# Kernel tuning notes

Hardware: AMD Instinct MI355X
Metric: run time of the kernel (lower is better)

## Reference

```python
import jax, jax.numpy as jnp
import numpy as np

NUM_NODES = 100000
NUM_EDGES = 640000
IN_DIM = 128
OUT_DIM = 128
NUM_REL = 16


def setup_inputs() -> dict:
    key = jax.random.key(0)
    k1, k2, k3, k4, k5 = jax.random.split(key, 5)
    x = jax.random.normal(k1, (NUM_NODES, IN_DIM), dtype=jnp.float32)
    edge_index = jax.random.randint(k2, (2, NUM_EDGES), 0, NUM_NODES, dtype=jnp.int64)
    edge_types = jax.random.randint(k3, (NUM_EDGES,), 0, NUM_REL, dtype=jnp.int64)
    # xavier-uniform-ish params
    rw_bound = float(np.sqrt(6.0 / (IN_DIM * OUT_DIM + NUM_REL)))
    relation_weights = jax.random.uniform(k4, (NUM_REL, IN_DIM, OUT_DIM), dtype=jnp.float32, minval=-rw_bound, maxval=rw_bound)
    sw_bound = float(np.sqrt(6.0 / (IN_DIM + OUT_DIM)))
    self_weight = jax.random.uniform(k5, (IN_DIM, OUT_DIM), dtype=jnp.float32, minval=-sw_bound, maxval=sw_bound)
    bias = jnp.zeros((OUT_DIM,), dtype=jnp.float32)
    return {
        'x': x,
        'edge_index': edge_index,
        'edge_types': edge_types,
        'relation_weights': relation_weights,
        'self_weight': self_weight,
        'bias': bias,
    }


def reference(x, edge_index, edge_types, relation_weights, self_weight, bias):
    num_nodes = x.shape[0]
    # self loop transform: (N, out)
    self_msg = x @ self_weight
    # transform all nodes by every relation weight once: (R, N, out)
    transformed = jnp.einsum('ni,rio->rno', x, relation_weights)
    src = edge_index[0]
    dst = edge_index[1]
    # per-edge message: pick (relation, source) transformed feature -> (E, out)
    msgs = transformed[edge_types, src]
    # scatter-add into destination nodes
    neighbor_msg = jax.ops.segment_sum(msgs, dst, num_segments=num_nodes)
    # dropout=0.0 (eval) -> identity
    return jax.nn.relu(self_msg + neighbor_msg + bias)
```

## Files before the change

### kernel.cpp

```cpp
#include <hip/hip_runtime.h>

#define N_NODES 100000
#define N_EDGES 640000
#define IN_DIM  128
#define OUT_DIM 128
#define N_REL   16
#define EPB     64
#define MEPB    128
#define SELF_PAD 100096
#define MAX_SLOTS (SELF_PAD + N_EDGES + 2048)
#define SENT    (N_EDGES + N_NODES)
#define MSG_ROWS (N_EDGES + N_NODES + 128)
#define NB_SCAN ((N_NODES + 255) / 256)
#define CVT_XB  (N_NODES * IN_DIM / 4 / 256)
#define CVT_WB  (17 * 16384 / 256)
#define HIST_B  ((N_EDGES + 255) / 256)
#define SELF_B  (SELF_PAD / 256)
#define MB      (MAX_SLOTS / MEPB)

typedef unsigned short u16;
typedef unsigned int   u32;
typedef __attribute__((ext_vector_type(8))) short bf16x8;
typedef __attribute__((ext_vector_type(4))) float f32x4;

__device__ inline u16 f2bf(float f) {
    u32 u = __builtin_bit_cast(u32, f);
    return (u16)((u + 0x7fffu + ((u >> 16) & 1u)) >> 16);
}
__device__ inline float bf2f(u16 s) {
    u32 u = ((u32)s) << 16;
    return __builtin_bit_cast(float, u);
}

__global__ __launch_bounds__(256) void k_pre(const float* __restrict__ x,
                                             const float* __restrict__ rw,
                                             const float* __restrict__ sw,
                                             const int* __restrict__ etype,
                                             const int* __restrict__ dst,
                                             u16* __restrict__ xb,
                                             u16* __restrict__ wt,
                                             int* __restrict__ counts_rel,
                                             int* __restrict__ dst_count,
                                             int* __restrict__ sorted) {
    int b = blockIdx.x, t = threadIdx.x;
    if (b < CVT_XB) {
        int i = b * 256 + t;
        float4 v = ((const float4*)x)[i];
        ushort4 p; p.x = f2bf(v.x); p.y = f2bf(v.y); p.z = f2bf(v.z); p.w = f2bf(v.w);
        ((ushort4*)xb)[i] = p;
    } else if (b < CVT_XB + CVT_WB) {
        int i = (b - CVT_XB) * 256 + t;
        int r = i >> 14, rem = i & 16383;
        int k = rem >> 7, np = rem & 127;
        float v = (r < 16) ? rw[i] : sw[rem];
        int c = np >> 4, nn = np & 15, kk = k >> 5, q = (k >> 3) & 3, j = k & 7;
        wt[(size_t)r * 16384 + (c * 4 + kk) * 512 + (q * 16 + nn) * 8 + j] = f2bf(v);
    } else if (b < CVT_XB + CVT_WB + HIST_B) {
        __shared__ int bins[N_REL];
        if (t < N_REL) bins[t] = 0;
        __syncthreads();
        int e = (b - CVT_XB - CVT_WB) * 256 + t;
        if (e < N_EDGES) {
            atomicAdd(&bins[etype[e]], 1);
            atomicAdd(&dst_count[dst[e]], 1);
        }
        __syncthreads();
        if (t < N_REL && bins[t]) atomicAdd(&counts_rel[t], bins[t]);
    } else {
        int i = (b - CVT_XB - CVT_WB - HIST_B) * 256 + t;
        sorted[i] = (i < N_NODES) ? (N_EDGES + i) : SENT;
    }
}

__global__ __launch_bounds__(256) void k_scan1(const int* __restrict__ dst_count,
                                               int* __restrict__ row_ptr,
                                               int* __restrict__ part) {
    __shared__ int buf[2][256];
    int t = threadIdx.x;
    int i = blockIdx.x * 256 + t;
    int v = (i < N_NODES) ? (dst_count[i] + 1) : 0;
    buf[0][t] = v;
    __syncthreads();
    int cur = 0;
    #pragma unroll
    for (int off = 1; off < 256; off <<= 1) {
        int nxt = cur ^ 1;
        int s = buf[cur][t];
        if (t >= off) s += buf[cur][t - off];
        buf[nxt][t] = s;
        __syncthreads();
        cur = nxt;
    }
    int inc = buf[cur][t];
    if (i < N_NODES) row_ptr[i] = inc - v;
    if (t == 255) part[blockIdx.x] = inc;
}

__global__ __launch_bounds__(512) void k_mid2(int* __restrict__ part,
                                              const int* __restrict__ counts,
                                              int* __restrict__ cursor,
                                              int* __restrict__ seg,
                                              int* __restrict__ sorted) {
    int t = threadIdx.x;
    if (blockIdx.x == 0) {
        __shared__ int buf[2][512];
        int v = (t < NB_SCAN) ? part[t] : 0;
        buf[0][t] = v;
        __syncthreads();
        int cur = 0;
        #pragma unroll
        for (int off = 1; off < 512; off <<= 1) {
            int nxt = cur ^ 1;
            int s = buf[cur][t];
            if (t >= off) s += buf[cur][t - off];
            buf[nxt][t] = s;
            __syncthreads();
            cur = nxt;
        }
        int inc = buf[cur][t];
        if (t < NB_SCAN) part[t] = inc - v;
    } else {
        __shared__ int s_seg[N_REL + 1];
        if (t == 0) {
            int s = SELF_PAD;
            for (int r = 0; r < N_REL; ++r) {
                cursor[r] = s; seg[r] = s; s_seg[r] = s;
                s += (counts[r] + 127) & ~127;
            }
            seg[N_REL] = s; s_seg[N_REL] = s;
        }
        __syncthreads();
        for (int r = 0; r < N_REL; ++r) {
            int b = s_seg[r] + counts[r], e2 = s_seg[r + 1];
            if (b + t < e2) sorted[b + t] = SENT;
        }
        for (int i = s_seg[N_REL] + t; i < MAX_SLOTS; i += 512)
            sorted[i] = SENT;
    }
}

__global__ __launch_bounds__(256) void k_scan3_scatter(int* __restrict__ row_ptr,
                                                       const int* __restrict__ part,
                                                       int* __restrict__ cursor_dst,
                                                       const int* __restrict__ etype,
                                                       int* __restrict__ cursor_rel,
                                                       int* __restrict__ sorted) {
    int t = threadIdx.x;
    if (blockIdx.x < NB_SCAN) {
        int i = blockIdx.x * 256 + t;
        if (i < N_NODES) {
            int r = row_ptr[i] + part[blockIdx.x];
            row_ptr[i] = r;
            cursor_dst[i] = r + 1;
        }
        if (i == 0) row_ptr[N_NODES] = N_EDGES + N_NODES;
    } else {
        __shared__ int bins[N_REL];
        __shared__ int base[N_REL];
        if (t < N_REL) bins[t] = 0;
        __syncthreads();
        int e = (blockIdx.x - NB_SCAN) * 256 + t;
        int rel = 0;
        bool valid = (e < N_EDGES);
        if (valid) { rel = etype[e]; atomicAdd(&bins[rel], 1); }
        __syncthreads();
        if (t < N_REL) {
            base[t] = bins[t] ? atomicAdd(&cursor_rel[t], bins[t]) : 0;
            bins[t] = 0;
        }
        __syncthreads();
        if (valid) {
            int p = atomicAdd(&bins[rel], 1);
            sorted[base[rel] + p] = e;
        }
    }
}

__global__ __launch_bounds__(256, 4) void k_msg_mfma(const u16* __restrict__ xb,
                                                     const u16* __restrict__ wt,
                                                     const int* __restrict__ src,
                                                     const int* __restrict__ etype,
                                                     const int* __restrict__ dst,
                                                     const int* __restrict__ sorted,
                                                     const int* __restrict__ row_ptr,
                                                     int* __restrict__ cursor_dst,
                                                     u16* __restrict__ msgs) {
    __shared__ u16 s_w[128 * 128];
    __shared__ int s_pos[MEPB];
    int t = threadIdx.x;
    const int q8 = MB >> 3, r8 = MB & 7;
    int xcd = blockIdx.x & 7, idx = blockIdx.x >> 3;
    int bid = (xcd < r8 ? xcd * (q8 + 1) : r8 * (q8 + 1) + (xcd - r8) * q8) + idx;
    int e0 = bid * MEPB;

    int ee0 = sorted[e0];
    if (ee0 >= SENT) return;
    int relb = (ee0 < N_EDGES) ? etype[ee0] : N_REL;

    int wv = t >> 6, lane = t & 63;
    int n = lane & 15, q = lane >> 4;
    int eb = wv * 32;

    bf16x8 bx[2][4];
    #pragma unroll
    for (int g = 0; g < 2; ++g) {
        int eid = sorted[e0 + eb + g * 16 + n];
        int sv = (eid < N_EDGES) ? src[eid]
               : (eid < SENT)    ? eid - N_EDGES : 0;
        const u16* xrow = xb + (size_t)sv * 128 + q * 8;
        #pragma unroll
        for (int kk = 0; kk < 4; ++kk)
            bx[g][kk] = *(const bf16x8*)(xrow + kk * 32);
    }

    const uint4* wsrc = (const uint4*)(wt + (size_t)relb * 16384);
    for (int i = t; i < 2048; i += 256)
        *(uint4*)&s_w[i * 8] = wsrc[i];

    if (t < MEPB) {
        int eid = sorted[e0 + t];
        int pv;
        if (eid < N_EDGES)   pv = atomicAdd(&cursor_dst[dst[eid]], 1);
        else if (eid < SENT) pv = row_ptr[eid - N_EDGES];
        else                 pv = SENT + ((e0 + t) & 127);
        s_pos[t] = pv;
    }
    __syncthreads();

    uint4 uv[2][4];
    #pragma unroll
    for (int c = 0; c < 8; ++c) {
        bf16x8 aw[4];
        #pragma unroll
        for (int kk = 0; kk < 4; ++kk)
            aw[kk] = *(const bf16x8*)&s_w[(c * 4 + kk) * 512 + lane * 8];
        #pragma unroll
        for (int g = 0; g < 2; ++g) {
            f32x4 acc = {0.f, 0.f, 0.f, 0.f};
            #pragma unroll
            for (int kk = 0; kk < 4; ++kk)
                acc = __builtin_amdgcn_mfma_f32_16x16x32_bf16(aw[kk], bx[g][kk], acc, 0, 0, 0);
            u32 lo = (u32)f2bf(acc[0]) | ((u32)f2bf(acc[1]) << 16);
            u32 hi = (u32)f2bf(acc[2]) | ((u32)f2bf(acc[3]) << 16);
            if ((c & 1) == 0) { uv[g][c >> 1].x = lo; uv[g][c >> 1].y = hi; }
            else              { uv[g][c >> 1].z = lo; uv[g][c >> 1].w = hi; }
        }
    }
    #pragma unroll
    for (int g = 0; g < 2; ++g) {
        int p = s_pos[eb + g * 16 + n];
        u32* mrow = (u32*)(msgs + (size_t)p * 128 + q * 32);
        #pragma unroll
        for (int j = 0; j < 4; ++j)
            *(uint4*)(mrow + j * 4) = uv[g][j];
    }
}

__global__ __launch_bounds__(256) void k_gather(const int* __restrict__ row_ptr,
                                                const u16* __restrict__ msgs,
                                                const float* __restrict__ bias,
                                                float* __restrict__ out) {
    int wid  = (blockIdx.x * 256 + threadIdx.x) >> 6;
    int lane = threadIdx.x & 63;
    if (wid >= N_NODES) return;
    int r0 = row_ptr[wid], r1 = row_ptr[wid + 1];
    int h = lane & 15, quarter = lane >> 4;
    const uint4* m = (const uint4*)msgs;
    float s[8] = {0.f,0.f,0.f,0.f,0.f,0.f,0.f,0.f};
    int i = r0 + quarter;
    for (; i + 4 < r1; i += 8) {
        uint4 v = m[(size_t)i * 16 + h];
        uint4 w = m[(size_t)(i + 4) * 16 + h];
        s[0] += bf2f((u16)(v.x & 0xffffu)); s[1] += bf2f((u16)(v.x >> 16));
        s[2] += bf2f((u16)(v.y & 0xffffu)); s[3] += bf2f((u16)(v.y >> 16));
        s[4] += bf2f((u16)(v.z & 0xffffu)); s[5] += bf2f((u16)(v.z >> 16));
        s[6] += bf2f((u16)(v.w & 0xffffu)); s[7] += bf2f((u16)(v.w >> 16));
        s[0] += bf2f((u16)(w.x & 0xffffu)); s[1] += bf2f((u16)(w.x >> 16));
        s[2] += bf2f((u16)(w.y & 0xffffu)); s[3] += bf2f((u16)(w.y >> 16));
        s[4] += bf2f((u16)(w.z & 0xffffu)); s[5] += bf2f((u16)(w.z >> 16));
        s[6] += bf2f((u16)(w.w & 0xffffu)); s[7] += bf2f((u16)(w.w >> 16));
    }
    if (i < r1) {
        uint4 v = m[(size_t)i * 16 + h];
        s[0] += bf2f((u16)(v.x & 0xffffu)); s[1] += bf2f((u16)(v.x >> 16));
        s[2] += bf2f((u16)(v.y & 0xffffu)); s[3] += bf2f((u16)(v.y >> 16));
        s[4] += bf2f((u16)(v.z & 0xffffu)); s[5] += bf2f((u16)(v.z >> 16));
        s[6] += bf2f((u16)(v.w & 0xffffu)); s[7] += bf2f((u16)(v.w >> 16));
    }
    #pragma unroll
    for (int j = 0; j < 8; ++j) {
        s[j] += __shfl_xor(s[j], 16);
        s[j] += __shfl_xor(s[j], 32);
    }
    if (quarter == 0) {
        int c0 = (2 * h) & 7, c1 = (2 * h + 1) & 7, qq = h >> 2;
        float4 b0 = *(const float4*)&bias[c0 * 16 + qq * 4];
        float4 b1 = *(const float4*)&bias[c1 * 16 + qq * 4];
        float* ob = out + (size_t)wid * 128;
        float4 v0, v1;
        v0.x = fmaxf(s[0] + b0.x, 0.f); v0.y = fmaxf(s[1] + b0.y, 0.f);
        v0.z = fmaxf(s[2] + b0.z, 0.f); v0.w = fmaxf(s[3] + b0.w, 0.f);
        v1.x = fmaxf(s[4] + b1.x, 0.f); v1.y = fmaxf(s[5] + b1.y, 0.f);
        v1.z = fmaxf(s[6] + b1.z, 0.f); v1.w = fmaxf(s[7] + b1.w, 0.f);
        *(float4*)(ob + c0 * 16 + qq * 4) = v0;
        *(float4*)(ob + c1 * 16 + qq * 4) = v1;
    }
}

__global__ __launch_bounds__(128) void k_self_old(const float* __restrict__ x,
                                                  const float* __restrict__ sw,
                                                  const float* __restrict__ bias,
                                                  float* __restrict__ out) {
    __shared__ float s_x[8][IN_DIM];
    int t = threadIdx.x;
    int n0 = blockIdx.x * 8;
    for (int i = t; i < 8 * IN_DIM; i += 128) {
        int r = i >> 7, j = i & 127;
        s_x[r][j] = x[(size_t)(n0 + r) * IN_DIM + j];
    }
    __syncthreads();
    float acc[8] = {0.f,0.f,0.f,0.f,0.f,0.f,0.f,0.f};
    for (int k = 0; k < IN_DIM; ++k) {
        float w = sw[k * OUT_DIM + t];
        #pragma unroll
        for (int i = 0; i < 8; ++i) acc[i] += s_x[i][k] * w;
    }
    float b = bias[t];
    #pragma unroll
    for (int i = 0; i < 8; ++i)
        out[(size_t)(n0 + i) * OUT_DIM + t] = acc[i] + b;
}

__global__ __launch_bounds__(256) void k_hist_rel(const int* __restrict__ etype,
                                                  int* __restrict__ counts_rel) {
    __shared__ int bins[N_REL];
    int t = threadIdx.x;
    if (t < N_REL) bins[t] = 0;
    __syncthreads();
    int e = blockIdx.x * 256 + t;
    if (e < N_EDGES) atomicAdd(&bins[etype[e]], 1);
    __syncthreads();
    if (t < N_REL && bins[t]) atomicAdd(&counts_rel[t], bins[t]);
}

__global__ void k_scan_rel(const int* __restrict__ counts, int* __restrict__ cursor) {
    if (threadIdx.x == 0) {
        int s = 0;
        for (int r = 0; r < N_REL; ++r) { cursor[r] = s; s += counts[r]; }
    }
}

__global__ __launch_bounds__(256) void k_scatter_rel(const int* __restrict__ etype,
                                                     int* __restrict__ cursor,
                                                     int* __restrict__ sorted) {
    __shared__ int bins[N_REL];
    __shared__ int base[N_REL];
    int t = threadIdx.x;
    if (t < N_REL) bins[t] = 0;
    __syncthreads();
    int e = blockIdx.x * 256 + t;
    int rel = 0;
    bool valid = (e < N_EDGES);
    if (valid) { rel = etype[e]; atomicAdd(&bins[rel], 1); }
    __syncthreads();
    if (t < N_REL) {
        base[t] = bins[t] ? atomicAdd(&cursor[t], bins[t]) : 0;
        bins[t] = 0;
    }
    __syncthreads();
    if (valid) {
        int p = atomicAdd(&bins[rel], 1);
        sorted[base[rel] + p] = e;
    }
}

__global__ __launch_bounds__(256) void k_edge_atomic(const float* __restrict__ x,
                                              const float* __restrict__ rw,
                                              const int* __restrict__ src,
                                              const int* __restrict__ dst,
                                              const int* __restrict__ etype,
                                              const int* __restrict__ sorted,
                                              float* __restrict__ out) {
    __shared__ int s_src[EPB], s_dst[EPB], s_rel[EPB];
    __shared__ float s_x[EPB][IN_DIM];
    int t = threadIdx.x;
    int e0 = blockIdx.x * EPB;
    if (t < EPB) {
        int eid = sorted[e0 + t];
        s_src[t] = src[eid]; s_dst[t] = dst[eid]; s_rel[t] = etype[eid];
    }
    __syncthreads();
    for (int i = t; i < EPB * IN_DIM; i += 256) {
        int e = i >> 7, j = i & 127;
        s_x[e][j] = x[(size_t)s_src[e] * IN_DIM + j];
    }
    int rel0 = s_rel[0];
    bool uni = true;
    for (int i = 1; i < EPB; ++i) uni &= (s_rel[i] == rel0);
    __syncthreads();
    int cg = t & 31, eg = t >> 5;
    for (int i = 0; i < 8; ++i) {
        int e = eg * 8 + i;
        int rel = uni ? rel0 : s_rel[e];
        const float4* Wr = (const float4*)(rw + (size_t)rel * IN_DIM * OUT_DIM);
        float a0=0.f, a1=0.f, a2=0.f, a3=0.f;
        for (int k = 0; k < 128; ++k) {
            float4 w = Wr[k * 32 + cg];
            float xv = s_x[e][k];
            a0 += xv * w.x; a1 += xv * w.y; a2 += xv * w.z; a3 += xv * w.w;
        }
        float* o = out + (size_t)s_dst[e] * OUT_DIM + cg * 4;
        atomicAdd(o + 0, a0); atomicAdd(o + 1, a1);
        atomicAdd(o + 2, a2); atomicAdd(o + 3, a3);
    }
}

__global__ void k_relu(float* __restrict__ out) {
    int i = blockIdx.x * blockDim.x + threadIdx.x;
    float4* o4 = (float4*)out;
    const int n4 = N_NODES * OUT_DIM / 4;
    if (i < n4) {
        float4 v = o4[i];
        v.x = fmaxf(v.x, 0.f); v.y = fmaxf(v.y, 0.f);
        v.z = fmaxf(v.z, 0.f); v.w = fmaxf(v.w, 0.f);
        o4[i] = v;
    }
}

extern "C" void kernel_launch(void* const* d_in, const int* in_sizes, int n_in,
                              void* d_out, int out_size, void* d_ws, size_t ws_size,
                              hipStream_t stream) {
    const float* x     = (const float*)d_in[0];
    const int*   eidx  = (const int*)d_in[1];
    const int*   etype = (const int*)d_in[2];
    const float* rw    = (const float*)d_in[3];
    const float* sw    = (const float*)d_in[4];
    const float* bias  = (const float*)d_in[5];
    float* out = (float*)d_out;
    const int* src = eidx;
    const int* dst = eidx + N_EDGES;

    int* counts_rel = (int*)d_ws;
    int* cursor_rel = counts_rel + 16;
    int* seg        = cursor_rel + 16;
    int* part       = seg + 32;
    int* dst_count  = part + 512;
    int* row_ptr    = dst_count + N_NODES;
    int* cursor_dst = row_ptr + N_NODES + 1;
    int* sorted     = cursor_dst + N_NODES;
    size_t off = (((char*)(sorted + MAX_SLOTS) - (char*)d_ws) + 255) & ~(size_t)255;
    u16* xb   = (u16*)((char*)d_ws + off);
    u16* wtb  = xb + (size_t)N_NODES * 128;
    u16* msgs = wtb + 17 * 16384;
    size_t need = (size_t)((char*)(msgs + (size_t)MSG_ROWS * 128) - (char*)d_ws);

    if (ws_size >= need) {
        hipMemsetAsync(d_ws, 0, (size_t)(576 + N_NODES) * sizeof(int), stream);
        k_pre<<<CVT_XB + CVT_WB + HIST_B + SELF_B, 256, 0, stream>>>(
            x, rw, sw, etype, dst, xb, wtb, counts_rel, dst_count, sorted);
        k_scan1<<<NB_SCAN, 256, 0, stream>>>(dst_count, row_ptr, part);
        k_mid2<<<2, 512, 0, stream>>>(part, counts_rel, cursor_rel, seg, sorted);
        k_scan3_scatter<<<NB_SCAN + HIST_B, 256, 0, stream>>>(
            row_ptr, part, cursor_dst, etype, cursor_rel, sorted);

        k_msg_mfma<<<MB, 256, 0, stream>>>(xb, wtb, src, etype, dst, sorted,
                                           row_ptr, cursor_dst, msgs);
        k_gather<<<(N_NODES * 64 + 255) / 256, 256, 0, stream>>>(row_ptr, msgs, bias, out);
    } else {
        hipMemsetAsync(counts_rel, 0, 16 * sizeof(int), stream);
        k_hist_rel<<<HIST_B, 256, 0, stream>>>(etype, counts_rel);
        k_scan_rel<<<1, 64, 0, stream>>>(counts_rel, cursor_rel);
        k_scatter_rel<<<HIST_B, 256, 0, stream>>>(etype, cursor_rel, sorted);
        k_self_old<<<N_NODES / 8, 128, 0, stream>>>(x, sw, bias, out);
        k_edge_atomic<<<N_EDGES / EPB, 256, 0, stream>>>(x, rw, src, dst, etype, sorted, out);
        k_relu<<<(N_NODES * OUT_DIM / 4 + 255) / 256, 256, 0, stream>>>(out);
    }
}
```

Baseline: 332.1 us.

## Write messages contiguously by relation slot and gather via per-destination slot indirection

The MFMA message kernel now writes each edge's transformed row to its relation-sorted slot, giving contiguous stores, instead of scattering rows to CSR-by-destination positions found with atomics. A separate edge_slots index is built during the scatter phase, which is now split from the row_ptr scan into its own kernel, so the gather kernel can locate each destination's messages. The XCD-aware block remapping is removed and the src lookup is staged through shared memory. In exchange the gather reads messages through one extra level of indirection, which makes those reads irregular, and one more kernel launch is added.

```diff
diff --git a/kernel.cpp b/kernel.cpp
--- a/kernel.cpp
+++ b/kernel.cpp
@@ -10,7 +10,6 @@
 #define SELF_PAD 100096
 #define MAX_SLOTS (SELF_PAD + N_EDGES + 2048)
 #define SENT    (N_EDGES + N_NODES)
-#define MSG_ROWS (N_EDGES + N_NODES + 128)
 #define NB_SCAN ((N_NODES + 255) / 256)
 #define CVT_XB  (N_NODES * IN_DIM / 4 / 256)
 #define CVT_WB  (17 * 16384 / 256)
@@ -139,40 +138,48 @@
     }
 }
 
-__global__ __launch_bounds__(256) void k_scan3_scatter(int* __restrict__ row_ptr,
-                                                       const int* __restrict__ part,
-                                                       int* __restrict__ cursor_dst,
-                                                       const int* __restrict__ etype,
-                                                       int* __restrict__ cursor_rel,
-                                                       int* __restrict__ sorted) {
-    int t = threadIdx.x;
-    if (blockIdx.x < NB_SCAN) {
-        int i = blockIdx.x * 256 + t;
-        if (i < N_NODES) {
-            int r = row_ptr[i] + part[blockIdx.x];
-            row_ptr[i] = r;
-            cursor_dst[i] = r + 1;
-        }
-        if (i == 0) row_ptr[N_NODES] = N_EDGES + N_NODES;
-    } else {
-        __shared__ int bins[N_REL];
-        __shared__ int base[N_REL];
-        if (t < N_REL) bins[t] = 0;
-        __syncthreads();
-        int e = (blockIdx.x - NB_SCAN) * 256 + t;
-        int rel = 0;
-        bool valid = (e < N_EDGES);
-        if (valid) { rel = etype[e]; atomicAdd(&bins[rel], 1); }
-        __syncthreads();
-        if (t < N_REL) {
-            base[t] = bins[t] ? atomicAdd(&cursor_rel[t], bins[t]) : 0;
-            bins[t] = 0;
-        }
-        __syncthreads();
-        if (valid) {
-            int p = atomicAdd(&bins[rel], 1);
-            sorted[base[rel] + p] = e;
-        }
+__global__ __launch_bounds__(256) void k_scan3(int* __restrict__ row_ptr,
+                                               const int* __restrict__ part,
+                                               int* __restrict__ cursor_dst,
+                                               int* __restrict__ edge_slots) {
+    int t = threadIdx.x;
+    int i = blockIdx.x * 256 + t;
+    if (i < N_NODES) {
+        int r = row_ptr[i] + part[blockIdx.x];
+        row_ptr[i] = r;
+        cursor_dst[i] = r + 1;
+        edge_slots[r] = i;
+    }
+    if (i == 0) row_ptr[N_NODES] = SENT;
+}
+
+__global__ __launch_bounds__(256) void k_scatter(const int* __restrict__ etype,
+                                                 const int* __restrict__ dst,
+                                                 int* __restrict__ cursor_rel,
+                                                 int* __restrict__ cursor_dst,
+                                                 int* __restrict__ sorted,
+                                                 int* __restrict__ edge_slots) {
+    __shared__ int bins[N_REL];
+    __shared__ int base[N_REL];
+    int t = threadIdx.x;
+    if (t < N_REL) bins[t] = 0;
+    __syncthreads();
+    int e = blockIdx.x * 256 + t;
+    int rel = 0;
+    bool valid = (e < N_EDGES);
+    if (valid) { rel = etype[e]; atomicAdd(&bins[rel], 1); }
+    __syncthreads();
+    if (t < N_REL) {
+        base[t] = bins[t] ? atomicAdd(&cursor_rel[t], bins[t]) : 0;
+        bins[t] = 0;
+    }
+    __syncthreads();
+    if (valid) {
+        int p = atomicAdd(&bins[rel], 1);
+        int slot = base[rel] + p;
+        sorted[slot] = e;
+        int pd = atomicAdd(&cursor_dst[dst[e]], 1);
+        edge_slots[pd] = slot;
     }
 }
 
@@ -180,52 +187,41 @@
                                                      const u16* __restrict__ wt,
                                                      const int* __restrict__ src,
                                                      const int* __restrict__ etype,
-                                                     const int* __restrict__ dst,
                                                      const int* __restrict__ sorted,
-                                                     const int* __restrict__ row_ptr,
-                                                     int* __restrict__ cursor_dst,
                                                      u16* __restrict__ msgs) {
     __shared__ u16 s_w[128 * 128];
-    __shared__ int s_pos[MEPB];
-    int t = threadIdx.x;
-    const int q8 = MB >> 3, r8 = MB & 7;
-    int xcd = blockIdx.x & 7, idx = blockIdx.x >> 3;
-    int bid = (xcd < r8 ? xcd * (q8 + 1) : r8 * (q8 + 1) + (xcd - r8) * q8) + idx;
-    int e0 = bid * MEPB;
+    __shared__ int s_src[MEPB];
+    int t = threadIdx.x;
+    int e0 = blockIdx.x * MEPB;
 
     int ee0 = sorted[e0];
     if (ee0 >= SENT) return;
     int relb = (ee0 < N_EDGES) ? etype[ee0] : N_REL;
+    const uint4* wsrc = (const uint4*)(wt + (size_t)relb * 16384);
+    for (int i = t; i < 2048; i += 256)
+        *(uint4*)&s_w[i * 8] = wsrc[i];
+    if (t < MEPB) {
+        int eid = sorted[e0 + t];
+        s_src[t] = (eid < N_EDGES) ? src[eid]
+                 : (eid < SENT)    ? eid - N_EDGES : -1;
+    }
+    __syncthreads();
 
     int wv = t >> 6, lane = t & 63;
     int n = lane & 15, q = lane >> 4;
     int eb = wv * 32;
 
     bf16x8 bx[2][4];
+    int sv[2];
     #pragma unroll
     for (int g = 0; g < 2; ++g) {
-        int eid = sorted[e0 + eb + g * 16 + n];
-        int sv = (eid < N_EDGES) ? src[eid]
-               : (eid < SENT)    ? eid - N_EDGES : 0;
-        const u16* xrow = xb + (size_t)sv * 128 + q * 8;
+        int en = eb + g * 16 + n;
+        sv[g] = s_src[en];
+        const u16* xrow = xb + (size_t)max(sv[g], 0) * 128 + q * 8;
         #pragma unroll
         for (int kk = 0; kk < 4; ++kk)
             bx[g][kk] = *(const bf16x8*)(xrow + kk * 32);
     }
-
-    const uint4* wsrc = (const uint4*)(wt + (size_t)relb * 16384);
-    for (int i = t; i < 2048; i += 256)
-        *(uint4*)&s_w[i * 8] = wsrc[i];
-
-    if (t < MEPB) {
-        int eid = sorted[e0 + t];
-        int pv;
-        if (eid < N_EDGES)   pv = atomicAdd(&cursor_dst[dst[eid]], 1);
-        else if (eid < SENT) pv = row_ptr[eid - N_EDGES];
-        else                 pv = SENT + ((e0 + t) & 127);
-        s_pos[t] = pv;
-    }
-    __syncthreads();
 
     uint4 uv[2][4];
     #pragma unroll
@@ -248,15 +244,17 @@
     }
     #pragma unroll
     for (int g = 0; g < 2; ++g) {
-        int p = s_pos[eb + g * 16 + n];
-        u32* mrow = (u32*)(msgs + (size_t)p * 128 + q * 32);
-        #pragma unroll
-        for (int j = 0; j < 4; ++j)
-            *(uint4*)(mrow + j * 4) = uv[g][j];
+        if (sv[g] >= 0) {
+            u32* mrow = (u32*)(msgs + (size_t)(e0 + eb + g * 16 + n) * 128 + q * 32);
+            #pragma unroll
+            for (int j = 0; j < 4; ++j)
+                *(uint4*)(mrow + j * 4) = uv[g][j];
+        }
     }
 }
 
 __global__ __launch_bounds__(256) void k_gather(const int* __restrict__ row_ptr,
+                                                const int* __restrict__ edge_slots,
                                                 const u16* __restrict__ msgs,
                                                 const float* __restrict__ bias,
                                                 float* __restrict__ out) {
@@ -269,8 +267,9 @@
     float s[8] = {0.f,0.f,0.f,0.f,0.f,0.f,0.f,0.f};
     int i = r0 + quarter;
     for (; i + 4 < r1; i += 8) {
-        uint4 v = m[(size_t)i * 16 + h];
-        uint4 w = m[(size_t)(i + 4) * 16 + h];
+        int s0 = edge_slots[i], s1 = edge_slots[i + 4];
+        uint4 v = m[(size_t)s0 * 16 + h];
+        uint4 w = m[(size_t)s1 * 16 + h];
         s[0] += bf2f((u16)(v.x & 0xffffu)); s[1] += bf2f((u16)(v.x >> 16));
         s[2] += bf2f((u16)(v.y & 0xffffu)); s[3] += bf2f((u16)(v.y >> 16));
         s[4] += bf2f((u16)(v.z & 0xffffu)); s[5] += bf2f((u16)(v.z >> 16));
@@ -281,7 +280,8 @@
         s[6] += bf2f((u16)(w.w & 0xffffu)); s[7] += bf2f((u16)(w.w >> 16));
     }
     if (i < r1) {
-        uint4 v = m[(size_t)i * 16 + h];
+        int s0 = edge_slots[i];
+        uint4 v = m[(size_t)s0 * 16 + h];
         s[0] += bf2f((u16)(v.x & 0xffffu)); s[1] += bf2f((u16)(v.x >> 16));
         s[2] += bf2f((u16)(v.y & 0xffffu)); s[3] += bf2f((u16)(v.y >> 16));
         s[4] += bf2f((u16)(v.z & 0xffffu)); s[5] += bf2f((u16)(v.z >> 16));
@@ -445,14 +445,15 @@
     int* seg        = cursor_rel + 16;
     int* part       = seg + 32;
     int* dst_count  = part + 512;
+    int* cursor_dst = dst_count;
     int* row_ptr    = dst_count + N_NODES;
-    int* cursor_dst = row_ptr + N_NODES + 1;
-    int* sorted     = cursor_dst + N_NODES;
-    size_t off = (((char*)(sorted + MAX_SLOTS) - (char*)d_ws) + 255) & ~(size_t)255;
+    int* sorted     = row_ptr + N_NODES + 1;
+    int* edge_slots = sorted + MAX_SLOTS;
+    size_t off = (((char*)(edge_slots + SENT) - (char*)d_ws) + 255) & ~(size_t)255;
     u16* xb   = (u16*)((char*)d_ws + off);
     u16* wtb  = xb + (size_t)N_NODES * 128;
     u16* msgs = wtb + 17 * 16384;
-    size_t need = (size_t)((char*)(msgs + (size_t)MSG_ROWS * 128) - (char*)d_ws);
+    size_t need = (size_t)((char*)(msgs + (size_t)MAX_SLOTS * 128) - (char*)d_ws);
 
     if (ws_size >= need) {
         hipMemsetAsync(d_ws, 0, (size_t)(576 + N_NODES) * sizeof(int), stream);
@@ -460,12 +461,12 @@
             x, rw, sw, etype, dst, xb, wtb, counts_rel, dst_count, sorted);
         k_scan1<<<NB_SCAN, 256, 0, stream>>>(dst_count, row_ptr, part);
         k_mid2<<<2, 512, 0, stream>>>(part, counts_rel, cursor_rel, seg, sorted);
-        k_scan3_scatter<<<NB_SCAN + HIST_B, 256, 0, stream>>>(
-            row_ptr, part, cursor_dst, etype, cursor_rel, sorted);
-
-        k_msg_mfma<<<MB, 256, 0, stream>>>(xb, wtb, src, etype, dst, sorted,
-                                           row_ptr, cursor_dst, msgs);
-        k_gather<<<(N_NODES * 64 + 255) / 256, 256, 0, stream>>>(row_ptr, msgs, bias, out);
+        k_scan3<<<NB_SCAN, 256, 0, stream>>>(row_ptr, part, cursor_dst, edge_slots);
+        k_scatter<<<HIST_B, 256, 0, stream>>>(etype, dst, cursor_rel, cursor_dst,
+                                              sorted, edge_slots);
+        k_msg_mfma<<<MB, 256, 0, stream>>>(xb, wtb, src, etype, sorted, msgs);
+        k_gather<<<(N_NODES * 64 + 255) / 256, 256, 0, stream>>>(
+            row_ptr, edge_slots, msgs, bias, out);
     } else {
         hipMemsetAsync(counts_rel, 0, 16 * sizeof(int), stream);
         k_hist_rel<<<HIST_B, 256, 0, stream>>>(etype, counts_rel);
```

Result: slower. 365.5 us (+10.1%).
